# Kernel optimization log

Measured on AMD Instinct MI355X. Metric: run time of the kernel, lower is better.

Reference implementation:

```python
import jax, jax.numpy as jnp
import numpy as np

N = 4_000_000   # batch size
L = 48          # number of stacked tiny layers
EPS = 1e-5      # BatchNorm1d default eps


def setup_inputs() -> dict:
    key = jax.random.key(0)
    ks = jax.random.split(key, 6)
    return {
        "x": jax.random.normal(ks[0], (N, 2), dtype=jnp.float32),
        "W": jax.random.normal(ks[1], (L, 2, 2), dtype=jnp.float32),
        "b": jax.random.normal(ks[2], (L, 2), dtype=jnp.float32) * 0.1,
        "gamma": jnp.ones((L, 2), dtype=jnp.float32),
        "beta": jnp.zeros((L, 2), dtype=jnp.float32),
        "scale": jax.random.normal(ks[3], (L, 2), dtype=jnp.float32),
        "shift": jax.random.normal(ks[4], (L, 2), dtype=jnp.float32) * 0.1,
        "Wf": jax.random.normal(ks[5], (1, 2), dtype=jnp.float32),
        "bf": jnp.zeros((1,), dtype=jnp.float32),
    }


def _forward(x, W, b, gamma, beta, scale, shift, Wf, bf):
    def layer_step(h, p):
        Wl, bl, gl, bel, scl, shl = p
        y = h @ Wl.T + bl                       # Linear(2,2)  -> [N,2]
        m = jnp.mean(y, axis=0)                 # BatchNorm1d (training stats)
        v = jnp.mean((y - m) ** 2, axis=0)      # biased variance
        y = (y - m) * jax.lax.rsqrt(v + EPS) * gl + bel
        y = jnp.tanh(y) * scl + shl             # Tanh + elementwise affine
        return y, None                          # dropout p=0 -> identity

    h, _ = jax.lax.scan(layer_step, x, (W, b, gamma, beta, scale, shift))
    return jax.nn.sigmoid(h @ Wf.T + bf)        # final Linear(2,1) + Sigmoid -> [N,1]


def reference(x, W, b, gamma, beta, scale, shift, Wf, bf):
    return _forward(x, W, b, gamma, beta, scale, shift, Wf, bf)
```

## Files before the change

### kernel.cpp

```cpp
#include <hip/hip_runtime.h>

#define NB   256
#define NT   1024
#define PRPT 8
#define TT   (NB * NT)

typedef unsigned long long ull;

struct alignas(128) Slot { double s[4]; double pad[12]; };

__device__ __forceinline__ float ex2(float x) { return __builtin_amdgcn_exp2f(x); }

__device__ __forceinline__ float rcp_acc(float d) {
  float r = __builtin_amdgcn_rcpf(d);
  return r * __builtin_fmaf(-d, r, 2.0f);
}
__device__ __forceinline__ float div_acc(float n, float d, float r) {
  float q = n * r;
  float rho = __builtin_fmaf(-q, d, n);
  return __builtin_fmaf(rho, r, q);
}

__device__ __forceinline__ float actf(float y, double P, double Q, float sc, float sh) {
  double u = fma((double)y, P, Q);
  float uf = (float)u;
  uf = fminf(fmaxf(uf, -60.0f), 60.0f);
  float e = ex2(uf);
  float den = e + 1.0f;
  float r = rcp_acc(den);
  float t = div_acc(e - 1.0f, den, r);
  return __builtin_fmaf(t, sc, sh);
}

__device__ __forceinline__ float sigm(double uo) {
  const double C1 = 1.4426950408889634074;
  float w = (float)(-uo * C1);
  w = fminf(fmaxf(w, -60.0f), 60.0f);
  float e = ex2(w);
  float d = 1.0f + e;
  float r = rcp_acc(d);
  return div_acc(1.0f, d, r);
}

__device__ __forceinline__ void layer_sync(
    int l, double s0, double s1, double s2, double s3,
    Slot* __restrict__ slot, Slot* __restrict__ coef,
    float gmv0, float gmv1, float btv0, float btv1, double dn,
    double& P0, double& P1, double& Q0, double& Q1)
{
  __shared__ double lr[NT / 64][4];
  __shared__ double lg[4][4];
  __shared__ double lc[4];
  const int lane = threadIdx.x & 63, wave = threadIdx.x >> 6;
  const ull pbit = (ull)((~((unsigned)l >> 1)) & 1u);

#pragma unroll
  for (int off = 32; off > 0; off >>= 1) {
    s0 += __shfl_down(s0, off, 64);
    s1 += __shfl_down(s1, off, 64);
    s2 += __shfl_down(s2, off, 64);
    s3 += __shfl_down(s3, off, 64);
  }
  if (lane == 0) { lr[wave][0] = s0; lr[wave][1] = s1; lr[wave][2] = s2; lr[wave][3] = s3; }
  __syncthreads();

  Slot* sb = slot + (size_t)(l & 1) * NB;
  if (threadIdx.x < NT / 64) {
    double a0 = lr[threadIdx.x][0], a1 = lr[threadIdx.x][1];
    double a2 = lr[threadIdx.x][2], a3 = lr[threadIdx.x][3];
#pragma unroll
    for (int off = 8; off > 0; off >>= 1) {
      a0 += __shfl_down(a0, off, 64);
      a1 += __shfl_down(a1, off, 64);
      a2 += __shfl_down(a2, off, 64);
      a3 += __shfl_down(a3, off, 64);
    }
    if (threadIdx.x == 0) {
      ull* my = (ull*)(sb + blockIdx.x)->s;
      __hip_atomic_store(my + 0, (__double_as_longlong(a0) & ~1ull) | pbit,
                         __ATOMIC_RELAXED, __HIP_MEMORY_SCOPE_AGENT);
      __hip_atomic_store(my + 1, (__double_as_longlong(a1) & ~1ull) | pbit,
                         __ATOMIC_RELAXED, __HIP_MEMORY_SCOPE_AGENT);
      __hip_atomic_store(my + 2, (__double_as_longlong(a2) & ~1ull) | pbit,
                         __ATOMIC_RELAXED, __HIP_MEMORY_SCOPE_AGENT);
      __hip_atomic_store(my + 3, (__double_as_longlong(a3) & ~1ull) | pbit,
                         __ATOMIC_RELAXED, __HIP_MEMORY_SCOPE_AGENT);
    }
  }

  if (blockIdx.x == 0) {
    if (threadIdx.x < NB) {
      ull* sl = (ull*)(sb + threadIdx.x)->s;
      ull v0, v1, v2, v3;
      for (;;) {
        v0 = __hip_atomic_load(sl + 0, __ATOMIC_RELAXED, __HIP_MEMORY_SCOPE_AGENT);
        v1 = __hip_atomic_load(sl + 1, __ATOMIC_RELAXED, __HIP_MEMORY_SCOPE_AGENT);
        v2 = __hip_atomic_load(sl + 2, __ATOMIC_RELAXED, __HIP_MEMORY_SCOPE_AGENT);
        v3 = __hip_atomic_load(sl + 3, __ATOMIC_RELAXED, __HIP_MEMORY_SCOPE_AGENT);
        if ((((v0 & v1 & v2 & v3) ^ pbit) & 1ull) == 0ull &&
            (((v0 | v1 | v2 | v3) ^ pbit) & 1ull) == 0ull) break;
        __builtin_amdgcn_s_sleep(1);
      }
      double g0 = __longlong_as_double((long long)v0);
      double g1 = __longlong_as_double((long long)v1);
      double g2 = __longlong_as_double((long long)v2);
      double g3 = __longlong_as_double((long long)v3);
#pragma unroll
      for (int off = 32; off > 0; off >>= 1) {
        g0 += __shfl_down(g0, off, 64);
        g1 += __shfl_down(g1, off, 64);
        g2 += __shfl_down(g2, off, 64);
        g3 += __shfl_down(g3, off, 64);
      }
      if (lane == 0) { lg[wave][0] = g0; lg[wave][1] = g1; lg[wave][2] = g2; lg[wave][3] = g3; }
    }
    __syncthreads();
    if (threadIdx.x == 0) {
      const double t0 = lg[0][0] + lg[1][0] + lg[2][0] + lg[3][0];
      const double t1 = lg[0][1] + lg[1][1] + lg[2][1] + lg[3][1];
      const double t2 = lg[0][2] + lg[1][2] + lg[2][2] + lg[3][2];
      const double t3 = lg[0][3] + lg[1][3] + lg[2][3] + lg[3][3];
      const double m0 = t0 * dn, m1 = t1 * dn;
      const double v0 = fma(-m0, m0, t2 * dn);
      const double v1 = fma(-m1, m1, t3 * dn);
      const double rs0 = 1.0 / sqrt(v0 + 1e-5);
      const double rs1 = 1.0 / sqrt(v1 + 1e-5);
      const double A0 = (double)gmv0 * rs0, A1 = (double)gmv1 * rs1;
      const double C2 = 2.8853900817779268147;
      const double p0 = A0 * C2, p1 = A1 * C2;
      const double q0 = ((double)btv0 - m0 * A0) * C2;
      const double q1 = ((double)btv1 - m1 * A1) * C2;
      ull* cl = (ull*)(coef + (l & 1))->s;
      __hip_atomic_store(cl + 0, (__double_as_longlong(p0) & ~1ull) | pbit,
                         __ATOMIC_RELAXED, __HIP_MEMORY_SCOPE_AGENT);
      __hip_atomic_store(cl + 1, (__double_as_longlong(p1) & ~1ull) | pbit,
                         __ATOMIC_RELAXED, __HIP_MEMORY_SCOPE_AGENT);
      __hip_atomic_store(cl + 2, (__double_as_longlong(q0) & ~1ull) | pbit,
                         __ATOMIC_RELAXED, __HIP_MEMORY_SCOPE_AGENT);
      __hip_atomic_store(cl + 3, (__double_as_longlong(q1) & ~1ull) | pbit,
                         __ATOMIC_RELAXED, __HIP_MEMORY_SCOPE_AGENT);
    }
  }

  if (threadIdx.x == 0) {
    ull* cl = (ull*)(coef + (l & 1))->s;
    ull v0, v1, v2, v3;
    for (;;) {
      v0 = __hip_atomic_load(cl + 0, __ATOMIC_RELAXED, __HIP_MEMORY_SCOPE_AGENT);
      v1 = __hip_atomic_load(cl + 1, __ATOMIC_RELAXED, __HIP_MEMORY_SCOPE_AGENT);
      v2 = __hip_atomic_load(cl + 2, __ATOMIC_RELAXED, __HIP_MEMORY_SCOPE_AGENT);
      v3 = __hip_atomic_load(cl + 3, __ATOMIC_RELAXED, __HIP_MEMORY_SCOPE_AGENT);
      if ((((v0 & v1 & v2 & v3) ^ pbit) & 1ull) == 0ull &&
          (((v0 | v1 | v2 | v3) ^ pbit) & 1ull) == 0ull) break;
    }
    lc[0] = __longlong_as_double((long long)v0);
    lc[1] = __longlong_as_double((long long)v1);
    lc[2] = __longlong_as_double((long long)v2);
    lc[3] = __longlong_as_double((long long)v3);
  }
  __syncthreads();
  P0 = lc[0]; P1 = lc[1]; Q0 = lc[2]; Q1 = lc[3];
}

__global__ __launch_bounds__(NT, 4) void fraud_persist(
    const float4* __restrict__ x, const float* __restrict__ W,
    const float* __restrict__ b, const float* __restrict__ gm,
    const float* __restrict__ bt, const float* __restrict__ sc,
    const float* __restrict__ sh, const float* __restrict__ Wf,
    const float* __restrict__ bf, float2* __restrict__ out,
    Slot* __restrict__ slot, Slot* __restrict__ coef, int N2, int L)
{
  const int tid = blockIdx.x * NT + threadIdx.x;
  float4 y[PRPT];
  double s0 = 0, s1 = 0, s2 = 0, s3 = 0;

  {
    const double w00 = W[0], w01 = W[1], w10 = W[2], w11 = W[3];
    const double b0 = b[0], b1 = b[1];
#pragma unroll
    for (int r = 0; r < PRPT; ++r) {
      const int i = tid + r * TT;
      const float4 p = (i < N2) ? x[i] : make_float4(0.f, 0.f, 0.f, 0.f);
      const double a0 = fma((double)p.x, w00, fma((double)p.y, w01, b0));
      const double a1 = fma((double)p.x, w10, fma((double)p.y, w11, b1));
      const double a2 = fma((double)p.z, w00, fma((double)p.w, w01, b0));
      const double a3 = fma((double)p.z, w10, fma((double)p.w, w11, b1));
      y[r] = make_float4((float)a0, (float)a1, (float)a2, (float)a3);
      if (i < N2) {
        s0 += a0 + a2; s1 += a1 + a3;
        s2 = fma(a0, a0, fma(a2, a2, s2));
        s3 = fma(a1, a1, fma(a3, a3, s3));
      }
    }
  }
  const double dn = 0.5 / (double)N2;

  float gmv0 = gm[0], gmv1 = gm[1], btv0 = bt[0], btv1 = bt[1];
  float sc0 = sc[0], sh0 = sh[0], sc1 = sc[1], sh1 = sh[1];
  double w00 = W[4], w01 = W[5], w10 = W[6], w11 = W[7];
  double bb0 = b[2], bb1 = b[3];

  double P0, P1, Q0, Q1;
  layer_sync(0, s0, s1, s2, s3, slot, coef, gmv0, gmv1, btv0, btv1, dn, P0, P1, Q0, Q1);

  for (int l = 0; l < L; ++l) {
    const bool last = (l == L - 1);
    const double cw00 = w00, cw01 = w01, cw10 = w10, cw11 = w11;
    const double cb0 = bb0, cb1 = bb1;
    const float csc0 = sc0, csh0 = sh0, csc1 = sc1, csh1 = sh1;

    s0 = 0; s1 = 0; s2 = 0; s3 = 0;
#pragma unroll
    for (int r = 0; r < PRPT; ++r) {
      const int i = tid + r * TT;
      const float z0 = actf(y[r].x, P0, Q0, csc0, csh0);
      const float z1 = actf(y[r].y, P1, Q1, csc1, csh1);
      const float z2 = actf(y[r].z, P0, Q0, csc0, csh0);
      const float z3 = actf(y[r].w, P1, Q1, csc1, csh1);
      if (!last) {
        const double a0 = fma((double)z0, cw00, fma((double)z1, cw01, cb0));
        const double a1 = fma((double)z0, cw10, fma((double)z1, cw11, cb1));
        const double a2 = fma((double)z2, cw00, fma((double)z3, cw01, cb0));
        const double a3 = fma((double)z2, cw10, fma((double)z3, cw11, cb1));
        y[r] = make_float4((float)a0, (float)a1, (float)a2, (float)a3);
        if (i < N2) {
          s0 += a0 + a2; s1 += a1 + a3;
          s2 = fma(a0, a0, fma(a2, a2, s2));
          s3 = fma(a1, a1, fma(a3, a3, s3));
        }
      } else if (i < N2) {
        const double u0 = fma((double)z0, cw00, fma((double)z1, cw01, cb0));
        const double u1 = fma((double)z2, cw00, fma((double)z3, cw01, cb0));
        out[i] = make_float2(sigm(u0), sigm(u1));
      }
    }
    if (!last) {
      const int n = l + 1;
      gmv0 = gm[2 * n]; gmv1 = gm[2 * n + 1];
      btv0 = bt[2 * n]; btv1 = bt[2 * n + 1];
      sc0 = sc[2 * n]; sh0 = sh[2 * n];
      sc1 = sc[2 * n + 1]; sh1 = sh[2 * n + 1];
      if (n < L - 1) {
        w00 = W[4 * n + 4]; w01 = W[4 * n + 5]; w10 = W[4 * n + 6]; w11 = W[4 * n + 7];
        bb0 = b[2 * n + 2]; bb1 = b[2 * n + 3];
      } else {
        w00 = Wf[0]; w01 = Wf[1]; w10 = 0.0; w11 = 0.0; bb0 = bf[0]; bb1 = 0.0;
      }
      layer_sync(n, s0, s1, s2, s3, slot, coef, gmv0, gmv1, btv0, btv1, dn,
                 P0, P1, Q0, Q1);
    }
  }
}

extern "C" void kernel_launch(void* const* d_in, const int* in_sizes, int n_in,
                              void* d_out, int out_size, void* d_ws, size_t ws_size,
                              hipStream_t stream) {
  const float* x  = (const float*)d_in[0];
  const float* W  = (const float*)d_in[1];
  const float* b  = (const float*)d_in[2];
  const float* gm = (const float*)d_in[3];
  const float* bt = (const float*)d_in[4];
  const float* sc = (const float*)d_in[5];
  const float* sh = (const float*)d_in[6];
  const float* Wf = (const float*)d_in[7];
  const float* bf = (const float*)d_in[8];
  const int N  = in_sizes[0] / 2;
  const int L  = in_sizes[1] / 4;
  const int N2 = N / 2;

  char* wsb = (char*)d_ws;
  Slot* coef = (Slot*)wsb;
  Slot* slot = (Slot*)(wsb + 4096);

  hipMemsetAsync(d_ws, 0, 4096 + 2 * NB * sizeof(Slot), stream);

  fraud_persist<<<NB, NT, 0, stream>>>(
      (const float4*)x, W, b, gm, bt, sc, sh, Wf, bf,
      (float2*)d_out, slot, coef, N2, L);
}
```

Before: 475.3 us.

## Replicate BatchNorm stat reduction across eight hub blocks to spread coefficient polling

Instead of block 0 alone reducing the per-block partial sums and publishing the normalization coefficients, eight hub blocks each redundantly reduce all partials and publish their own copy. Non-hub blocks poll the copy belonging to their hub (blockIdx mod 8), and hubs use their locally computed coefficients directly. This aims to cut contention and latency on the single coefficient cache line at each of the 48 grid-wide barriers. The cost is eight times the reads of the partial-sum slots per layer and a coefficient buffer that must now be large enough for 2×8 slots.

Measured after the change: 465.0 us. -2.2%, faster.

```diff
diff --git a/kernel.cpp b/kernel.cpp
--- a/kernel.cpp
+++ b/kernel.cpp
@@ -4,6 +4,7 @@
 #define NT   1024
 #define PRPT 8
 #define TT   (NB * NT)
+#define NHUB 8
 
 typedef unsigned long long ull;
 
@@ -88,7 +89,7 @@
     }
   }
 
-  if (blockIdx.x == 0) {
+  if (blockIdx.x < NHUB) {
     if (threadIdx.x < NB) {
       ull* sl = (ull*)(sb + threadIdx.x)->s;
       ull v0, v1, v2, v3;
@@ -127,36 +128,37 @@
       const double rs1 = 1.0 / sqrt(v1 + 1e-5);
       const double A0 = (double)gmv0 * rs0, A1 = (double)gmv1 * rs1;
       const double C2 = 2.8853900817779268147;
-      const double p0 = A0 * C2, p1 = A1 * C2;
-      const double q0 = ((double)btv0 - m0 * A0) * C2;
-      const double q1 = ((double)btv1 - m1 * A1) * C2;
-      ull* cl = (ull*)(coef + (l & 1))->s;
-      __hip_atomic_store(cl + 0, (__double_as_longlong(p0) & ~1ull) | pbit,
-                         __ATOMIC_RELAXED, __HIP_MEMORY_SCOPE_AGENT);
-      __hip_atomic_store(cl + 1, (__double_as_longlong(p1) & ~1ull) | pbit,
-                         __ATOMIC_RELAXED, __HIP_MEMORY_SCOPE_AGENT);
-      __hip_atomic_store(cl + 2, (__double_as_longlong(q0) & ~1ull) | pbit,
-                         __ATOMIC_RELAXED, __HIP_MEMORY_SCOPE_AGENT);
-      __hip_atomic_store(cl + 3, (__double_as_longlong(q1) & ~1ull) | pbit,
-                         __ATOMIC_RELAXED, __HIP_MEMORY_SCOPE_AGENT);
-    }
-  }
-
-  if (threadIdx.x == 0) {
-    ull* cl = (ull*)(coef + (l & 1))->s;
-    ull v0, v1, v2, v3;
-    for (;;) {
-      v0 = __hip_atomic_load(cl + 0, __ATOMIC_RELAXED, __HIP_MEMORY_SCOPE_AGENT);
-      v1 = __hip_atomic_load(cl + 1, __ATOMIC_RELAXED, __HIP_MEMORY_SCOPE_AGENT);
-      v2 = __hip_atomic_load(cl + 2, __ATOMIC_RELAXED, __HIP_MEMORY_SCOPE_AGENT);
-      v3 = __hip_atomic_load(cl + 3, __ATOMIC_RELAXED, __HIP_MEMORY_SCOPE_AGENT);
-      if ((((v0 & v1 & v2 & v3) ^ pbit) & 1ull) == 0ull &&
-          (((v0 | v1 | v2 | v3) ^ pbit) & 1ull) == 0ull) break;
-    }
-    lc[0] = __longlong_as_double((long long)v0);
-    lc[1] = __longlong_as_double((long long)v1);
-    lc[2] = __longlong_as_double((long long)v2);
-    lc[3] = __longlong_as_double((long long)v3);
+      const ull w0 = (__double_as_longlong(A0 * C2) & ~1ull) | pbit;
+      const ull w1 = (__double_as_longlong(A1 * C2) & ~1ull) | pbit;
+      const ull w2 = (__double_as_longlong(((double)btv0 - m0 * A0) * C2) & ~1ull) | pbit;
+      const ull w3 = (__double_as_longlong(((double)btv1 - m1 * A1) * C2) & ~1ull) | pbit;
+      ull* cl = (ull*)(coef + (size_t)(l & 1) * NHUB + blockIdx.x)->s;
+      __hip_atomic_store(cl + 0, w0, __ATOMIC_RELAXED, __HIP_MEMORY_SCOPE_AGENT);
+      __hip_atomic_store(cl + 1, w1, __ATOMIC_RELAXED, __HIP_MEMORY_SCOPE_AGENT);
+      __hip_atomic_store(cl + 2, w2, __ATOMIC_RELAXED, __HIP_MEMORY_SCOPE_AGENT);
+      __hip_atomic_store(cl + 3, w3, __ATOMIC_RELAXED, __HIP_MEMORY_SCOPE_AGENT);
+      lc[0] = __longlong_as_double((long long)w0);
+      lc[1] = __longlong_as_double((long long)w1);
+      lc[2] = __longlong_as_double((long long)w2);
+      lc[3] = __longlong_as_double((long long)w3);
+    }
+  } else {
+    if (threadIdx.x == 0) {
+      ull* cl = (ull*)(coef + (size_t)(l & 1) * NHUB + (blockIdx.x & (NHUB - 1)))->s;
+      ull v0, v1, v2, v3;
+      for (;;) {
+        v0 = __hip_atomic_load(cl + 0, __ATOMIC_RELAXED, __HIP_MEMORY_SCOPE_AGENT);
+        v1 = __hip_atomic_load(cl + 1, __ATOMIC_RELAXED, __HIP_MEMORY_SCOPE_AGENT);
+        v2 = __hip_atomic_load(cl + 2, __ATOMIC_RELAXED, __HIP_MEMORY_SCOPE_AGENT);
+        v3 = __hip_atomic_load(cl + 3, __ATOMIC_RELAXED, __HIP_MEMORY_SCOPE_AGENT);
+        if ((((v0 & v1 & v2 & v3) ^ pbit) & 1ull) == 0ull &&
+            (((v0 | v1 | v2 | v3) ^ pbit) & 1ull) == 0ull) break;
+      }
+      lc[0] = __longlong_as_double((long long)v0);
+      lc[1] = __longlong_as_double((long long)v1);
+      lc[2] = __longlong_as_double((long long)v2);
+      lc[3] = __longlong_as_double((long long)v3);
+    }
   }
   __syncthreads();
   P0 = lc[0]; P1 = lc[1]; Q0 = lc[2]; Q1 = lc[3];
```
